# Kernel tuning notes

Hardware: AMD Instinct MI355X
Metric: run time of the kernel (lower is better)

Reference implementation:

```python
import jax, jax.numpy as jnp
import numpy as np

N = 100000   # n_nodes
E = 1600000  # n_edges (avg degree 16)
IN, HID, OUT = 128, 128, 64


def setup_inputs() -> dict:
    key = jax.random.key(0)
    k0, k1, k2, k3 = jax.random.split(key, 4)
    x = jax.random.normal(k0, (N, IN), dtype=jnp.float32)
    edge_index = jax.random.randint(k1, (2, E), 0, N, dtype=jnp.int32)
    # Glorot-ish init for GCNConv weights, zero bias (PyG default bias=True)
    W1 = jax.random.normal(k2, (IN, HID), dtype=jnp.float32) * (1.0 / np.sqrt(IN))
    b1 = jnp.zeros((HID,), dtype=jnp.float32)
    W2 = jax.random.normal(k3, (HID, OUT), dtype=jnp.float32) * (1.0 / np.sqrt(HID))
    b2 = jnp.zeros((OUT,), dtype=jnp.float32)
    return {"x": x, "W1": W1, "b1": b1, "W2": W2, "b2": b2, "edge_index": edge_index}


def gcn_layer(x, W, b, src, dst):
    """PyG GCNConv: add self-loops, symmetric deg^{-1/2} normalization,
    linear transform, scatter-add aggregation at dst, plus bias."""
    n = x.shape[0]
    h = x @ W                                   # [n, d_out]
    loops = jnp.arange(n, dtype=src.dtype)
    s = jnp.concatenate([src, loops])           # sources incl. self-loops
    d = jnp.concatenate([dst, loops])           # targets incl. self-loops
    deg = jax.ops.segment_sum(jnp.ones_like(d, dtype=h.dtype), d, num_segments=n)
    dinv = jnp.where(deg > 0, jax.lax.rsqrt(deg), 0.0)
    norm = dinv[s] * dinv[d]                    # [E+n]
    msg = h[s] * norm[:, None]                  # gather + scale
    out = jax.ops.segment_sum(msg, d, num_segments=n)  # scatter-add
    return out + b


def reference(x, W1, b1, W2, b2, edge_index):
    src, dst = edge_index[0], edge_index[1]
    h = jax.nn.relu(gcn_layer(x, W1, b1, src, dst))
    return gcn_layer(h, W2, b2, src, dst)
```

## Files before the change

### kernel.cpp

```cpp
#include <hip/hip_runtime.h>

#define NNODES 100000
#define NEDGES 1600000
#define IND 128
#define HIDD 128
#define OUTD 64

#define BSHIFT 9
#define BSIZE  512
#define NBUCK  ((NNODES + BSIZE - 1) / BSIZE)
#define SLACK  9216
#define BIN_EPB  2048
#define SEG_CAP  10240
#define BINB   ((NEDGES + BIN_EPB - 1) / BIN_EPB)
#define WTB    ((IND * HIDD + HIDD * OUTD + 255) / 256)
#define GEMMB  ((NNODES + 127) / 128)

typedef unsigned int  uint32;
typedef __attribute__((ext_vector_type(8))) short short8;
typedef __attribute__((ext_vector_type(4))) float floatx4;
typedef __attribute__((ext_vector_type(4))) unsigned int uivec4;
typedef __attribute__((ext_vector_type(4))) float fvec4;

__device__ __forceinline__ unsigned short f2bf(float f) {
    union { float f; uint32 u; } x; x.f = f;
    uint32 u = x.u;
    return (unsigned short)((u + 0x7fffu + ((u >> 16) & 1u)) >> 16);
}
__device__ __forceinline__ float bflo(uint32 u) {
    union { uint32 i; float f; } x; x.i = u << 16; return x.f;
}
__device__ __forceinline__ float bfhi(uint32 u) {
    union { uint32 i; float f; } x; x.i = u & 0xffff0000u; return x.f;
}

__global__ void k_bin(const int* __restrict__ src, const int* __restrict__ dst,
                      int* __restrict__ bcnt, uint32* __restrict__ staging, int e,
                      const float* __restrict__ W1, const float* __restrict__ W2,
                      unsigned short* __restrict__ wt1, unsigned short* __restrict__ wt2) {
    const int tid = threadIdx.x;
    if (blockIdx.x >= BINB) {
        int idx = (blockIdx.x - BINB) * 256 + tid;
        if (idx < IND * HIDD) {
            int k = idx / HIDD, m = idx - k * HIDD;
            wt1[m * IND + k] = f2bf(W1[idx]);
        } else {
            int j = idx - IND * HIDD;
            if (j < HIDD * OUTD) {
                int k = j / OUTD, m = j - k * OUTD;
                wt2[m * HIDD + k] = f2bf(W2[j]);
            }
        }
        return;
    }

    __shared__ int lh[NBUCK];
    __shared__ int lcur[NBUCK];
    for (int i = tid; i < NBUCK; i += 256) lh[i] = 0;
    __syncthreads();

    int start = blockIdx.x * BIN_EPB;
    int end = min(start + BIN_EPB, e);

    for (int i = start + tid; i < end; i += 256)
        atomicAdd(&lh[dst[i] >> BSHIFT], 1);
    __syncthreads();

    for (int i = tid; i < NBUCK; i += 256)
        lcur[i] = lh[i] ? atomicAdd(&bcnt[i], lh[i]) : 0;
    __syncthreads();

    for (int i = start + tid; i < end; i += 256) {
        int d = dst[i], s = src[i];
        int b = d >> BSHIFT;
        int pos = atomicAdd(&lcur[b], 1);
        if (pos < SLACK)
            staging[b * SLACK + pos] = ((uint32)(d & (BSIZE - 1)) << 17) | (uint32)s;
    }
}

__global__ __launch_bounds__(512)
void k_fill3(const uint32* __restrict__ staging, const int* __restrict__ bcnt,
             int* __restrict__ row_ptr, int* __restrict__ csr_src,
             float* __restrict__ dinv, int n) {
    __shared__ int nc[512];
    __shared__ int lcur[512];
    __shared__ int sbuf[512];
    __shared__ int seg[SEG_CAP];
    const int b = blockIdx.x;
    const int base = b << BSHIFT;
    const int tid = threadIdx.x;
    const int v = base + tid;

    nc[tid] = 0;

    int vb = (tid < NBUCK) ? bcnt[tid] : 0;
    sbuf[tid] = vb;
    __syncthreads();
    for (int off = 1; off < 512; off <<= 1) {
        int t = (tid >= off) ? sbuf[tid - off] : 0;
        __syncthreads();
        sbuf[tid] += t;
        __syncthreads();
    }
    const int r0    = (b > 0) ? sbuf[b - 1] : 0;
    const int total = sbuf[NBUCK - 1];
    __syncthreads();

    const uint32* st = staging + (size_t)b * SLACK;
    const int cnt = bcnt[b];
    for (int i = tid; i < cnt; i += 512)
        atomicAdd(&nc[st[i] >> 17], 1);
    __syncthreads();

    int dg = nc[tid];
    sbuf[tid] = dg;
    __syncthreads();
    for (int off = 1; off < 512; off <<= 1) {
        int t = (tid >= off) ? sbuf[tid - off] : 0;
        __syncthreads();
        sbuf[tid] += t;
        __syncthreads();
    }
    int ex = sbuf[tid] - dg;
    if (v < n) {
        row_ptr[v] = r0 + ex;
        dinv[v] = rsqrtf((float)(dg + 1));
    }
    lcur[tid] = ex;
    if (b == NBUCK - 1 && tid == 0) row_ptr[n] = total;
    __syncthreads();

    for (int i = tid; i < cnt; i += 512) {
        uint32 p = st[i];
        int dl = (int)(p >> 17);
        int s  = (int)(p & 0x1FFFFu);
        int pos = atomicAdd(&lcur[dl], 1);
        if (pos < SEG_CAP) seg[pos] = s;
        else               csr_src[r0 + pos] = s;
    }
    __syncthreads();
    int lim = min(cnt, SEG_CAP);
    for (int i = tid; i < lim; i += 512) csr_src[r0 + i] = seg[i];
}

template<int K, int M, bool ABF16>
__launch_bounds__(512)
__global__ void gemm_mfma(const void* __restrict__ Ap, const unsigned short* __restrict__ WT,
                          const float* __restrict__ dinv, unsigned short* __restrict__ C, int n) {
    constexpr int KP = K + 8;
    constexpr int NT = M / 16;
    __shared__ unsigned short Asl[128 * KP];
    __shared__ unsigned short Wsl[M * KP];

    const int tid = threadIdx.x;
    const int row0 = blockIdx.x * 128;

    {
        constexpr int SEG = (K * 2) / 16;
        const uint4* srcp = (const uint4*)WT;
        for (int idx = tid; idx < M * SEG; idx += 512) {
            int r = idx / SEG, s = idx - r * SEG;
            *(uint4*)(Wsl + r * KP + s * 8) = srcp[idx];
        }
    }
    if constexpr (ABF16) {
        constexpr int U4R = K / 8;
        const unsigned short* Ab = (const unsigned short*)Ap;
        for (int idx = tid; idx < 128 * U4R; idx += 512) {
            int r = idx / U4R, s = idx - r * U4R;
            int grow = row0 + r; if (grow >= n) grow = n - 1;
            *(uint4*)(Asl + r * KP + s * 8) = *(const uint4*)(Ab + (size_t)grow * K + s * 8);
        }
    } else {
        constexpr int F4R = K / 4;
        const float* Af = (const float*)Ap;
        for (int idx = tid; idx < 128 * F4R; idx += 512) {
            int r = idx / F4R, s = idx - r * F4R;
            int grow = row0 + r; if (grow >= n) grow = n - 1;
            float4 v = *(const float4*)(Af + (size_t)grow * K + s * 4);
            uint32 p0 = (uint32)f2bf(v.x) | ((uint32)f2bf(v.y) << 16);
            uint32 p1 = (uint32)f2bf(v.z) | ((uint32)f2bf(v.w) << 16);
            *(uint2*)(Asl + r * KP + s * 4) = make_uint2(p0, p1);
        }
    }
    __syncthreads();

    const int lane = tid & 63;
    const int wave = tid >> 6;
    const int mm = lane & 15;
    const int qq = lane >> 4;

    floatx4 acc[NT];
#pragma unroll
    for (int t = 0; t < NT; t++) acc[t] = (floatx4){0.f, 0.f, 0.f, 0.f};

#pragma unroll
    for (int kc = 0; kc < K / 32; kc++) {
        short8 a = *(const short8*)(Asl + (wave * 16 + mm) * KP + kc * 32 + qq * 8);
#pragma unroll
        for (int t = 0; t < NT; t++) {
            short8 b = *(const short8*)(Wsl + (t * 16 + mm) * KP + kc * 32 + qq * 8);
            acc[t] = __builtin_amdgcn_mfma_f32_16x16x32_bf16(a, b, acc[t], 0, 0, 0);
        }
    }

#pragma unroll
    for (int r = 0; r < 4; r++) {
        int grow = row0 + wave * 16 + qq * 4 + r;
        if (grow < n) {
            float dv = dinv[grow];
#pragma unroll
            for (int t = 0; t < NT; t++)
                C[(size_t)grow * M + t * 16 + mm] = f2bf(acc[t][r] * dv);
        }
    }
}

__launch_bounds__(256)
__global__ void gather_gemm(const unsigned short* __restrict__ h,
                            const int* __restrict__ row_ptr,
                            const int* __restrict__ csr_src,
                            const float* __restrict__ dinv,
                            const float* __restrict__ bias1,
                            const unsigned short* __restrict__ WT2,
                            unsigned short* __restrict__ C2, int n) {
    constexpr int K  = HIDD;
    constexpr int KP = K + 8;
    constexpr int M2 = OUTD;
    __shared__ unsigned short Atl[16 * KP];
    __shared__ unsigned short Wsl[M2 * KP];

    const int tid = threadIdx.x;

    {
        constexpr int SEG = (K * 2) / 16;
        const uint4* srcp = (const uint4*)WT2;
        for (int idx = tid; idx < M2 * SEG; idx += 256) {
            int r = idx / SEG, s = idx - r * SEG;
            *(uint4*)(Wsl + r * KP + s * 8) = srcp[idx];
        }
    }

    const int g = tid >> 4;
    const int l = tid & 15;
    const int v0 = blockIdx.x * 16;
    const int v = v0 + g;

    uint4 pk = make_uint4(0u, 0u, 0u, 0u);
    if (v < n) {
        const float dv = dinv[v];
        float acc[8];
        {
            uint4 u = *(const uint4*)(h + (size_t)v * K + l * 8);
            acc[0] = bflo(u.x); acc[1] = bfhi(u.x);
            acc[2] = bflo(u.y); acc[3] = bfhi(u.y);
            acc[4] = bflo(u.z); acc[5] = bfhi(u.z);
            acc[6] = bflo(u.w); acc[7] = bfhi(u.w);
        }

        int j   = row_ptr[v];
        int end = row_ptr[v + 1];
        for (; j + 3 < end; j += 4) {
            int s0 = csr_src[j];
            int s1 = csr_src[j + 1];
            int s2 = csr_src[j + 2];
            int s3 = csr_src[j + 3];
            uint4 u0 = *(const uint4*)(h + (size_t)s0 * K + l * 8);
            uint4 u1 = *(const uint4*)(h + (size_t)s1 * K + l * 8);
            uint4 u2 = *(const uint4*)(h + (size_t)s2 * K + l * 8);
            uint4 u3 = *(const uint4*)(h + (size_t)s3 * K + l * 8);
            acc[0] += (bflo(u0.x) + bflo(u1.x)) + (bflo(u2.x) + bflo(u3.x));
            acc[1] += (bfhi(u0.x) + bfhi(u1.x)) + (bfhi(u2.x) + bfhi(u3.x));
            acc[2] += (bflo(u0.y) + bflo(u1.y)) + (bflo(u2.y) + bflo(u3.y));
            acc[3] += (bfhi(u0.y) + bfhi(u1.y)) + (bfhi(u2.y) + bfhi(u3.y));
            acc[4] += (bflo(u0.z) + bflo(u1.z)) + (bflo(u2.z) + bflo(u3.z));
            acc[5] += (bfhi(u0.z) + bfhi(u1.z)) + (bfhi(u2.z) + bfhi(u3.z));
            acc[6] += (bflo(u0.w) + bflo(u1.w)) + (bflo(u2.w) + bflo(u3.w));
            acc[7] += (bfhi(u0.w) + bfhi(u1.w)) + (bfhi(u2.w) + bfhi(u3.w));
        }
        for (; j < end; j++) {
            int s0 = csr_src[j];
            uint4 u0 = *(const uint4*)(h + (size_t)s0 * K + l * 8);
            acc[0] += bflo(u0.x); acc[1] += bfhi(u0.x);
            acc[2] += bflo(u0.y); acc[3] += bfhi(u0.y);
            acc[4] += bflo(u0.z); acc[5] += bfhi(u0.z);
            acc[6] += bflo(u0.w); acc[7] += bfhi(u0.w);
        }

#pragma unroll
        for (int i = 0; i < 8; i++) {
            acc[i] = fmaxf(acc[i] * dv + bias1[l * 8 + i], 0.0f);
        }
        pk.x = (uint32)f2bf(acc[0]) | ((uint32)f2bf(acc[1]) << 16);
        pk.y = (uint32)f2bf(acc[2]) | ((uint32)f2bf(acc[3]) << 16);
        pk.z = (uint32)f2bf(acc[4]) | ((uint32)f2bf(acc[5]) << 16);
        pk.w = (uint32)f2bf(acc[6]) | ((uint32)f2bf(acc[7]) << 16);
    }
    *(uint4*)(Atl + g * KP + l * 8) = pk;
    __syncthreads();

    const int lane = tid & 63;
    const int wv = tid >> 6;
    const int mm = lane & 15;
    const int qq = lane >> 4;

    floatx4 o = (floatx4){0.f, 0.f, 0.f, 0.f};
#pragma unroll
    for (int kc = 0; kc < K / 32; kc++) {
        short8 a = *(const short8*)(Atl + mm * KP + kc * 32 + qq * 8);
        short8 b = *(const short8*)(Wsl + (wv * 16 + mm) * KP + kc * 32 + qq * 8);
        o = __builtin_amdgcn_mfma_f32_16x16x32_bf16(a, b, o, 0, 0, 0);
    }

#pragma unroll
    for (int r = 0; r < 4; r++) {
        int grow = v0 + qq * 4 + r;
        if (grow < n) {
            float dv2 = dinv[grow];
            C2[(size_t)grow * M2 + wv * 16 + mm] = f2bf(o[r] * dv2);
        }
    }
}

template<int M, bool RELU, bool OBF16>
__launch_bounds__(256)
__global__ void gather_k(const unsigned short* __restrict__ h,
                         const int* __restrict__ row_ptr,
                         const int* __restrict__ csr_src,
                         const float* __restrict__ dinv,
                         const float* __restrict__ bias,
                         void* __restrict__ outp, int n) {
    constexpr int LPG = M / 8;
    constexpr int GPB = 256 / LPG;
    const int g = threadIdx.x / LPG;
    const int l = threadIdx.x % LPG;
    const int v = blockIdx.x * GPB + g;
    if (v >= n) return;

    const float dv = dinv[v];
    float acc[8];
    {
        uint4 u = *(const uint4*)(h + (size_t)v * M + l * 8);
        acc[0] = bflo(u.x); acc[1] = bfhi(u.x);
        acc[2] = bflo(u.y); acc[3] = bfhi(u.y);
        acc[4] = bflo(u.z); acc[5] = bfhi(u.z);
        acc[6] = bflo(u.w); acc[7] = bfhi(u.w);
    }

    int j   = row_ptr[v];
    int end = row_ptr[v + 1];
    for (; j + 3 < end; j += 4) {
        int s0 = csr_src[j];
        int s1 = csr_src[j + 1];
        int s2 = csr_src[j + 2];
        int s3 = csr_src[j + 3];
        uint4 u0 = *(const uint4*)(h + (size_t)s0 * M + l * 8);
        uint4 u1 = *(const uint4*)(h + (size_t)s1 * M + l * 8);
        uint4 u2 = *(const uint4*)(h + (size_t)s2 * M + l * 8);
        uint4 u3 = *(const uint4*)(h + (size_t)s3 * M + l * 8);
        acc[0] += (bflo(u0.x) + bflo(u1.x)) + (bflo(u2.x) + bflo(u3.x));
        acc[1] += (bfhi(u0.x) + bfhi(u1.x)) + (bfhi(u2.x) + bfhi(u3.x));
        acc[2] += (bflo(u0.y) + bflo(u1.y)) + (bflo(u2.y) + bflo(u3.y));
        acc[3] += (bfhi(u0.y) + bfhi(u1.y)) + (bfhi(u2.y) + bfhi(u3.y));
        acc[4] += (bflo(u0.z) + bflo(u1.z)) + (bflo(u2.z) + bflo(u3.z));
        acc[5] += (bfhi(u0.z) + bfhi(u1.z)) + (bfhi(u2.z) + bfhi(u3.z));
        acc[6] += (bflo(u0.w) + bflo(u1.w)) + (bflo(u2.w) + bflo(u3.w));
        acc[7] += (bfhi(u0.w) + bfhi(u1.w)) + (bfhi(u2.w) + bfhi(u3.w));
    }
    for (; j < end; j++) {
        int s0 = csr_src[j];
        uint4 u0 = *(const uint4*)(h + (size_t)s0 * M + l * 8);
        acc[0] += bflo(u0.x); acc[1] += bfhi(u0.x);
        acc[2] += bflo(u0.y); acc[3] += bfhi(u0.y);
        acc[4] += bflo(u0.z); acc[5] += bfhi(u0.z);
        acc[6] += bflo(u0.w); acc[7] += bfhi(u0.w);
    }

#pragma unroll
    for (int i = 0; i < 8; i++) {
        acc[i] = acc[i] * dv + bias[l * 8 + i];
        if (RELU) acc[i] = fmaxf(acc[i], 0.0f);
    }

    if constexpr (OBF16) {
        uivec4 p;
#pragma unroll
        for (int c = 0; c < 4; c++)
            p[c] = (uint32)f2bf(acc[2 * c]) | ((uint32)f2bf(acc[2 * c + 1]) << 16);
        __builtin_nontemporal_store(p,
            (uivec4*)((unsigned short*)outp + (size_t)v * M + l * 8));
    } else {
        float* op = (float*)outp + (size_t)v * M + l * 8;
        fvec4 a0 = {acc[0], acc[1], acc[2], acc[3]};
        fvec4 a1 = {acc[4], acc[5], acc[6], acc[7]};
        __builtin_nontemporal_store(a0, (fvec4*)op);
        __builtin_nontemporal_store(a1, (fvec4*)(op + 4));
    }
}

extern "C" void kernel_launch(void* const* d_in, const int* in_sizes, int n_in,
                              void* d_out, int out_size, void* d_ws, size_t ws_size,
                              hipStream_t stream) {
    const float* x  = (const float*)d_in[0];
    const float* W1 = (const float*)d_in[1];
    const float* b1 = (const float*)d_in[2];
    const float* W2 = (const float*)d_in[3];
    const float* b2 = (const float*)d_in[4];
    const int*   ei = (const int*)d_in[5];
    const int* src = ei;
    const int* dst = ei + NEDGES;
    float* out = (float*)d_out;

    char* ws = (char*)d_ws;
    float*  dinv    = (float*)ws;   ws += (size_t)NNODES * 4;
    int*    row_ptr = (int*)ws;     ws += (size_t)(NNODES + 4) * 4;
    int*    bcnt    = (int*)ws;     ws += 256 * 4;
    unsigned short* wt1 = (unsigned short*)ws;  ws += (size_t)IND * HIDD * 2;
    unsigned short* wt2 = (unsigned short*)ws;  ws += (size_t)HIDD * OUTD * 2;
    int*    csr_src = (int*)ws;     ws += (size_t)NEDGES * 4;
    uint32* staging = (uint32*)ws;  ws += (size_t)NBUCK * SLACK * 4;
    unsigned short* hbf1 = (unsigned short*)ws; ws += (size_t)NNODES * HIDD * 2;
    unsigned short* hbf2 = (unsigned short*)ws;

    hipMemsetAsync(bcnt, 0, 256 * 4, stream);
    k_bin<<<BINB + WTB, 256, 0, stream>>>(src, dst, bcnt, staging, NEDGES, W1, W2, wt1, wt2);
    k_fill3<<<NBUCK, 512, 0, stream>>>(staging, bcnt, row_ptr, csr_src, dinv, NNODES);

    gemm_mfma<IND, HIDD, false><<<GEMMB, 512, 0, stream>>>(
        x, wt1, dinv, hbf1, NNODES);

    gather_gemm<<<(NNODES + 15) / 16, 256, 0, stream>>>(
        hbf1, row_ptr, csr_src, dinv, b1, wt2, hbf2, NNODES);

    gather_k<OUTD, false, false><<<(NNODES * (OUTD / 8) + 255) / 256, 256, 0, stream>>>(
        hbf2, row_ptr, csr_src, dinv, b2, out, NNODES);
}
```

Baseline: 310.1 us.

## Halve CSR bucket size, vectorize edge binning, and use wave-shuffle scans

Bucket size drops from 512 to 256 nodes, which doubles the number of CSR-fill blocks (391 instead of 196) and shrinks each block's shared staging segment. The binning kernel now loads four int4 vectors of src/dst per thread and processes 4096 edges per block. The fill kernel replaces its two Hillis-Steele block scans with a reduction over preceding bucket counts and a wave-level shuffle scan. The aim is more parallelism and fewer barriers in CSR construction. In exchange, the staging slack per bucket is tighter, which raises overflow risk on skewed degree distributions.

Result: faster. 289.3 us (-6.7%).

```diff
diff --git a/kernel.cpp b/kernel.cpp
--- a/kernel.cpp
+++ b/kernel.cpp
@@ -6,12 +6,12 @@
 #define HIDD 128
 #define OUTD 64
 
-#define BSHIFT 9
-#define BSIZE  512
+#define BSHIFT 8
+#define BSIZE  256
 #define NBUCK  ((NNODES + BSIZE - 1) / BSIZE)
-#define SLACK  9216
-#define BIN_EPB  2048
-#define SEG_CAP  10240
+#define SLACK  4800
+#define SEG_CAP 5120
+#define BIN_EPB 4096
 #define BINB   ((NEDGES + BIN_EPB - 1) / BIN_EPB)
 #define WTB    ((IND * HIDD + HIDD * OUTD + 255) / 256)
 #define GEMMB  ((NNODES + 127) / 128)
@@ -59,79 +59,114 @@
     for (int i = tid; i < NBUCK; i += 256) lh[i] = 0;
     __syncthreads();
 
-    int start = blockIdx.x * BIN_EPB;
-    int end = min(start + BIN_EPB, e);
-
-    for (int i = start + tid; i < end; i += 256)
-        atomicAdd(&lh[dst[i] >> BSHIFT], 1);
+    const int start = blockIdx.x * BIN_EPB;
+    const int4* d4 = (const int4*)dst;
+    const int4* s4 = (const int4*)src;
+
+    int4 dv[4], sv[4];
+    bool val[4];
+#pragma unroll
+    for (int k = 0; k < 4; k++) {
+        int off = start + 4 * (k * 256 + tid);
+        val[k] = off < e;
+        if (val[k]) { dv[k] = d4[off >> 2]; sv[k] = s4[off >> 2]; }
+    }
+
+#pragma unroll
+    for (int k = 0; k < 4; k++) {
+        if (val[k]) {
+            atomicAdd(&lh[dv[k].x >> BSHIFT], 1);
+            atomicAdd(&lh[dv[k].y >> BSHIFT], 1);
+            atomicAdd(&lh[dv[k].z >> BSHIFT], 1);
+            atomicAdd(&lh[dv[k].w >> BSHIFT], 1);
+        }
+    }
     __syncthreads();
 
     for (int i = tid; i < NBUCK; i += 256)
         lcur[i] = lh[i] ? atomicAdd(&bcnt[i], lh[i]) : 0;
     __syncthreads();
 
-    for (int i = start + tid; i < end; i += 256) {
-        int d = dst[i], s = src[i];
-        int b = d >> BSHIFT;
-        int pos = atomicAdd(&lcur[b], 1);
-        if (pos < SLACK)
-            staging[b * SLACK + pos] = ((uint32)(d & (BSIZE - 1)) << 17) | (uint32)s;
-    }
-}
-
-__global__ __launch_bounds__(512)
+#pragma unroll
+    for (int k = 0; k < 4; k++) {
+        if (val[k]) {
+            int d, s, b, pos;
+            d = dv[k].x; s = sv[k].x; b = d >> BSHIFT;
+            pos = atomicAdd(&lcur[b], 1);
+            if (pos < SLACK) staging[b * SLACK + pos] = ((uint32)(d & (BSIZE - 1)) << 17) | (uint32)s;
+            d = dv[k].y; s = sv[k].y; b = d >> BSHIFT;
+            pos = atomicAdd(&lcur[b], 1);
+            if (pos < SLACK) staging[b * SLACK + pos] = ((uint32)(d & (BSIZE - 1)) << 17) | (uint32)s;
+            d = dv[k].z; s = sv[k].z; b = d >> BSHIFT;
+            pos = atomicAdd(&lcur[b], 1);
+            if (pos < SLACK) staging[b * SLACK + pos] = ((uint32)(d & (BSIZE - 1)) << 17) | (uint32)s;
+            d = dv[k].w; s = sv[k].w; b = d >> BSHIFT;
+            pos = atomicAdd(&lcur[b], 1);
+            if (pos < SLACK) staging[b * SLACK + pos] = ((uint32)(d & (BSIZE - 1)) << 17) | (uint32)s;
+        }
+    }
+}
+
+__global__ __launch_bounds__(256)
 void k_fill3(const uint32* __restrict__ staging, const int* __restrict__ bcnt,
              int* __restrict__ row_ptr, int* __restrict__ csr_src,
              float* __restrict__ dinv, int n) {
-    __shared__ int nc[512];
-    __shared__ int lcur[512];
-    __shared__ int sbuf[512];
+    __shared__ int nc[BSIZE];
+    __shared__ int lcur[BSIZE];
+    __shared__ int red[256];
+    __shared__ int wsum[4];
     __shared__ int seg[SEG_CAP];
     const int b = blockIdx.x;
     const int base = b << BSHIFT;
     const int tid = threadIdx.x;
-    const int v = base + tid;
 
     nc[tid] = 0;
 
-    int vb = (tid < NBUCK) ? bcnt[tid] : 0;
-    sbuf[tid] = vb;
-    __syncthreads();
-    for (int off = 1; off < 512; off <<= 1) {
-        int t = (tid >= off) ? sbuf[tid - off] : 0;
+    int t0 = (tid < b) ? bcnt[tid] : 0;
+    int t1 = (tid + 256 < b) ? bcnt[tid + 256] : 0;
+    red[tid] = t0 + t1;
+    __syncthreads();
+    for (int off = 128; off > 0; off >>= 1) {
+        if (tid < off) red[tid] += red[tid + off];
         __syncthreads();
-        sbuf[tid] += t;
-        __syncthreads();
-    }
-    const int r0    = (b > 0) ? sbuf[b - 1] : 0;
-    const int total = sbuf[NBUCK - 1];
-    __syncthreads();
+    }
+    const int r0 = red[0];
 
     const uint32* st = staging + (size_t)b * SLACK;
     const int cnt = bcnt[b];
-    for (int i = tid; i < cnt; i += 512)
+    for (int i = tid; i < cnt; i += 256)
         atomicAdd(&nc[st[i] >> 17], 1);
     __syncthreads();
 
+    const int lane = tid & 63;
+    const int w = tid >> 6;
     int dg = nc[tid];
-    sbuf[tid] = dg;
-    __syncthreads();
-    for (int off = 1; off < 512; off <<= 1) {
-        int t = (tid >= off) ? sbuf[tid - off] : 0;
-        __syncthreads();
-        sbuf[tid] += t;
-        __syncthreads();
-    }
-    int ex = sbuf[tid] - dg;
-    if (v < n) {
-        row_ptr[v] = r0 + ex;
-        dinv[v] = rsqrtf((float)(dg + 1));
+    int v = dg;
+#pragma unroll
+    for (int off = 1; off < 64; off <<= 1) {
+        int t = __shfl_up(v, off);
+        if (lane >= off) v += t;
+    }
+    if (lane == 63) wsum[w] = v;
+    __syncthreads();
+    if (tid == 0) {
+        int a = 0;
+#pragma unroll
+        for (int i = 0; i < 4; i++) { int t = wsum[i]; wsum[i] = a; a += t; }
+    }
+    __syncthreads();
+    const int inc = v + wsum[w];
+    const int ex = inc - dg;
+    const int vnode = base + tid;
+    if (vnode < n) {
+        row_ptr[vnode] = r0 + ex;
+        dinv[vnode] = rsqrtf((float)(dg + 1));
     }
     lcur[tid] = ex;
-    if (b == NBUCK - 1 && tid == 0) row_ptr[n] = total;
-    __syncthreads();
-
-    for (int i = tid; i < cnt; i += 512) {
+    if (b == NBUCK - 1 && tid == 255) row_ptr[n] = r0 + inc;
+    __syncthreads();
+
+    for (int i = tid; i < cnt; i += 256) {
         uint32 p = st[i];
         int dl = (int)(p >> 17);
         int s  = (int)(p & 0x1FFFFu);
@@ -141,7 +176,7 @@
     }
     __syncthreads();
     int lim = min(cnt, SEG_CAP);
-    for (int i = tid; i < lim; i += 512) csr_src[r0 + i] = seg[i];
+    for (int i = tid; i < lim; i += 256) csr_src[r0 + i] = seg[i];
 }
 
 template<int K, int M, bool ABF16>
@@ -415,7 +450,7 @@
     char* ws = (char*)d_ws;
     float*  dinv    = (float*)ws;   ws += (size_t)NNODES * 4;
     int*    row_ptr = (int*)ws;     ws += (size_t)(NNODES + 4) * 4;
-    int*    bcnt    = (int*)ws;     ws += 256 * 4;
+    int*    bcnt    = (int*)ws;     ws += 512 * 4;
     unsigned short* wt1 = (unsigned short*)ws;  ws += (size_t)IND * HIDD * 2;
     unsigned short* wt2 = (unsigned short*)ws;  ws += (size_t)HIDD * OUTD * 2;
     int*    csr_src = (int*)ws;     ws += (size_t)NEDGES * 4;
@@ -423,9 +458,9 @@
     unsigned short* hbf1 = (unsigned short*)ws; ws += (size_t)NNODES * HIDD * 2;
     unsigned short* hbf2 = (unsigned short*)ws;
 
-    hipMemsetAsync(bcnt, 0, 256 * 4, stream);
+    hipMemsetAsync(bcnt, 0, 512 * 4, stream);
     k_bin<<<BINB + WTB, 256, 0, stream>>>(src, dst, bcnt, staging, NEDGES, W1, W2, wt1, wt2);
-    k_fill3<<<NBUCK, 512, 0, stream>>>(staging, bcnt, row_ptr, csr_src, dinv, NNODES);
+    k_fill3<<<NBUCK, 256, 0, stream>>>(staging, bcnt, row_ptr, csr_src, dinv, NNODES);
 
     gemm_mfma<IND, HIDD, false><<<GEMMB, 512, 0, stream>>>(
         x, wt1, dinv, hbf1, NNODES);
```
